# Kernel optimization log

Measured on AMD Instinct MI355X. Metric: run time of the kernel, lower is better.

## Reference

```python
import jax, jax.numpy as jnp
import numpy as np

N_EXPERTS = 8
D_MODEL = 1024
D_FF = 2048
N_TOKENS = 4096
TOP_K = 2


def _init_expert_weight(key, shape):
    # matches torch init: bound = sqrt(3) * (sqrt(1/3)/sqrt(fan_in)) = 1/sqrt(fan_in)
    fan_in = shape[1]
    bound = 1.0 / np.sqrt(fan_in)
    return jax.random.uniform(key, shape, dtype=jnp.float32, minval=-bound, maxval=bound)


def setup_inputs() -> dict:
    key = jax.random.key(0)
    k_x, k_idx, k_w, k1, k2, k3 = jax.random.split(key, 6)
    x = jax.random.normal(k_x, (N_TOKENS, D_MODEL), dtype=jnp.float32)
    expert_indices = jax.random.randint(k_idx, (N_TOKENS, TOP_K), 0, N_EXPERTS)
    expert_weights = jax.random.uniform(k_w, (N_TOKENS, TOP_K), dtype=jnp.float32)
    w1 = _init_expert_weight(k1, (N_EXPERTS, D_MODEL, D_FF))
    w2 = _init_expert_weight(k2, (N_EXPERTS, D_MODEL, D_FF))
    w3 = _init_expert_weight(k3, (N_EXPERTS, D_FF, D_MODEL))
    return {"x": x, "expert_indices": expert_indices, "expert_weights": expert_weights,
            "w1": w1, "w2": w2, "w3": w3}


def reference(x, expert_indices, expert_weights, w1, w2, w3):
    # SwiGLU per expert, computed densely over all (token, expert) pairs,
    # then the top-k selected expert outputs are gathered and combined.
    # Mathematically identical to the padded-bmm dispatch/combine in the source.
    gate = jax.nn.silu(jnp.einsum('td,edf->tef', x, w1))   # [T, E, F]
    value = jnp.einsum('td,edf->tef', x, w2)               # [T, E, F]
    hidden = gate * value                                  # [T, E, F]
    out_e = jnp.einsum('tef,efd->ted', hidden, w3)         # [T, E, D]
    # gather each token's top-k expert outputs: [T, K, D]
    sel = jnp.take_along_axis(out_e, expert_indices[:, :, None], axis=1)
    return jnp.sum(sel * expert_weights[:, :, None], axis=1)  # [T, D]
```

## Files before the change

### kernel.cpp

```cpp
#include <hip/hip_runtime.h>
#include <hip/hip_bf16.h>

#define N_TOK   4096
#define DM      1024
#define DF      2048
#define NEXP    8
#define NPAIR   (N_TOK * 2)
#define BM      128
#define BN      128
#define BK      32

typedef __attribute__((ext_vector_type(8))) short bf16x8;
typedef __attribute__((ext_vector_type(4))) float f32x4;

__device__ __forceinline__ unsigned short to_bf16(float f) {
    unsigned u = __builtin_bit_cast(unsigned, f);
    unsigned r = (u + 0x7FFFu + ((u >> 16) & 1u)) >> 16;
    return (unsigned short)r;
}
__device__ __forceinline__ unsigned pk_bf16(float a, float b) {
    return (unsigned)to_bf16(a) | ((unsigned)to_bf16(b) << 16);
}
__device__ __forceinline__ void gld16(const unsigned short* g, unsigned short* l) {
    __builtin_amdgcn_global_load_lds(
        (const __attribute__((address_space(1))) unsigned int*)(g),
        (__attribute__((address_space(3))) unsigned int*)(l), 16, 0, 0);
}

__global__ void k_count(const int* __restrict__ eidx, int* __restrict__ meta) {
    int i = blockIdx.x * 256 + threadIdx.x;
    if (i < NPAIR) atomicAdd(&meta[eidx[i] & 7], 1);
}
__global__ void k_scan(int* __restrict__ meta) {
    if (threadIdx.x == 0) {
        int off = 0, mt = 0;
        for (int e = 0; e < NEXP; ++e) {
            meta[16 + e] = off; meta[25 + e] = mt;
            int c = meta[e];
            off += c; mt += (c + BM - 1) / BM;
        }
        meta[16 + NEXP] = off; meta[25 + NEXP] = mt; meta[34] = mt;
    }
}
__global__ void k_scatter(const int* __restrict__ eidx, int* __restrict__ meta,
                          int* __restrict__ rows) {
    int i = blockIdx.x * 256 + threadIdx.x;
    if (i < NPAIR) {
        int e = eidx[i] & 7;
        int p = meta[16 + e] + atomicAdd(&meta[8 + e], 1);
        rows[p] = i;
    }
}

__global__ __launch_bounds__(256)
void k_cvt_x(const float* __restrict__ x, unsigned short* __restrict__ xb) {
    int i = (blockIdx.x * 256 + threadIdx.x) * 8;
    float4 v0 = *(const float4*)(x + i);
    float4 v1 = *(const float4*)(x + i + 4);
    uint4 w;
    w.x = pk_bf16(v0.x, v0.y); w.y = pk_bf16(v0.z, v0.w);
    w.z = pk_bf16(v1.x, v1.y); w.w = pk_bf16(v1.z, v1.w);
    *(uint4*)(xb + i) = w;
}

__global__ __launch_bounds__(256)
void k_transpose(const float* __restrict__ src, unsigned short* __restrict__ dst,
                 int K, int F) {
    __shared__ __align__(16) unsigned short tile[64 * 80];
    const int e  = blockIdx.z;
    const int k0 = blockIdx.y * 64;
    const int f0 = blockIdx.x * 64;
    const int t  = threadIdx.x;
    const float* s = src + (size_t)e * K * F;
    unsigned short* d = dst + (size_t)e * K * F;
    const int fi = t & 63;
    const int kg = t >> 6;
    #pragma unroll
    for (int i = 0; i < 16; ++i) {
        int k = kg * 16 + i;
        tile[k * 80 + fi] = to_bf16(s[(size_t)(k0 + k) * F + f0 + fi]);
    }
    __syncthreads();
    const int kc = (t & 7) * 8;
    const int fo = t >> 3;
    #pragma unroll
    for (int j = 0; j < 2; ++j) {
        int f = fo + j * 32;
        unsigned short v[8];
        #pragma unroll
        for (int i = 0; i < 8; ++i) v[i] = tile[(kc + i) * 80 + f];
        uint4 w;
        w.x = (unsigned)v[0] | ((unsigned)v[1] << 16);
        w.y = (unsigned)v[2] | ((unsigned)v[3] << 16);
        w.z = (unsigned)v[4] | ((unsigned)v[5] << 16);
        w.w = (unsigned)v[6] | ((unsigned)v[7] << 16);
        *(uint4*)&d[(size_t)(f0 + f) * K + k0 + kc] = w;
    }
}

__global__ __launch_bounds__(256, 2)
void k_gemm1_bf(const unsigned short* __restrict__ xb,
                const unsigned short* __restrict__ w1t,
                const unsigned short* __restrict__ w2t,
                const int* __restrict__ meta,
                const int* __restrict__ rows,
                unsigned short* __restrict__ H)
{
    __shared__ __align__(16) unsigned short L[3][12288];
    __shared__ int s_tok[BM];

    const int mt = blockIdx.y;
    if (mt >= meta[34]) return;
    int e = 0;
    #pragma unroll
    for (int i = 0; i < NEXP - 1; ++i) if (mt >= meta[25 + i + 1]) e = i + 1;
    const int rowEnd = meta[16 + e + 1];
    const int row0   = meta[16 + e] + (mt - meta[25 + e]) * BM;
    const int f0     = blockIdx.x * BN;
    const int tid    = threadIdx.x;

    if (tid < BM) {
        int gr = row0 + tid;
        s_tok[tid] = (gr < rowEnd) ? (rows[gr] >> 1) : 0;
    }
    __syncthreads();

    const int lane = tid & 63;
    const int wave = tid >> 6;
    const int r0 = wave * 32 + (lane >> 2);
    const int r1 = r0 + 16;
    const int kb = (lane & 3) * 8;
    const unsigned short* a_src0 = xb + (size_t)s_tok[r0] * DM + kb;
    const unsigned short* a_src1 = xb + (size_t)s_tok[r1] * DM + kb;
    const size_t wb = (size_t)e * DM * DF;
    const unsigned short* b1_src0 = w1t + wb + (size_t)(f0 + r0) * DM + kb;
    const unsigned short* b1_src1 = w1t + wb + (size_t)(f0 + r1) * DM + kb;
    const unsigned short* b2_src0 = w2t + wb + (size_t)(f0 + r0) * DM + kb;
    const unsigned short* b2_src1 = w2t + wb + (size_t)(f0 + r1) * DM + kb;

    f32x4 accg[4][4], accv[4][4];
    #pragma unroll
    for (int i = 0; i < 4; ++i)
        #pragma unroll
        for (int j = 0; j < 4; ++j) { accg[i][j] = (f32x4)0.f; accv[i][j] = (f32x4)0.f; }

    const int wm = (wave >> 1) * 64;
    const int wn = (wave & 1) * 64;
    const int am = lane & 15;
    const int ak = (lane >> 4) * 8;

    auto stage = [&](int b, int k0) {
        unsigned short* base = &L[b][0] + wave * 1024;
        gld16(a_src0  + k0, base);
        gld16(a_src1  + k0, base + 512);
        gld16(b1_src0 + k0, base + 4096);
        gld16(b1_src1 + k0, base + 4608);
        gld16(b2_src0 + k0, base + 8192);
        gld16(b2_src1 + k0, base + 8704);
    };
    auto compute = [&](int b) {
        const unsigned short* Ab = &L[b][0];
        bf16x8 a[4], b1[4], b2[4];
        #pragma unroll
        for (int mi = 0; mi < 4; ++mi)
            a[mi] = *(const bf16x8*)&Ab[(wm + mi * 16 + am) * BK + ak];
        #pragma unroll
        for (int ni = 0; ni < 4; ++ni) {
            b1[ni] = *(const bf16x8*)&Ab[4096 + (wn + ni * 16 + am) * BK + ak];
            b2[ni] = *(const bf16x8*)&Ab[8192 + (wn + ni * 16 + am) * BK + ak];
        }
        #pragma unroll
        for (int mi = 0; mi < 4; ++mi)
            #pragma unroll
            for (int ni = 0; ni < 4; ++ni) {
                accg[mi][ni] = __builtin_amdgcn_mfma_f32_16x16x32_bf16(a[mi], b1[ni], accg[mi][ni], 0, 0, 0);
                accv[mi][ni] = __builtin_amdgcn_mfma_f32_16x16x32_bf16(a[mi], b2[ni], accv[mi][ni], 0, 0, 0);
            }
    };

    stage(0, 0);
    stage(1, BK);
    for (int t = 0; t < DM / BK; ++t) {
        const int b = t % 3;
        if (t < DM / BK - 2) {
            stage((t + 2) % 3, (t + 2) * BK);
            asm volatile("s_waitcnt vmcnt(12)" ::: "memory");
        } else if (t == DM / BK - 2) {
            asm volatile("s_waitcnt vmcnt(6)" ::: "memory");
        } else {
            asm volatile("s_waitcnt vmcnt(0)" ::: "memory");
        }
        __builtin_amdgcn_s_barrier();
        __builtin_amdgcn_sched_barrier(0);
        compute(b);
        __builtin_amdgcn_sched_barrier(0);
        __builtin_amdgcn_s_barrier();
    }

    const int cn = lane & 15;
    const int cq = (lane >> 4) * 4;
    #pragma unroll
    for (int mi = 0; mi < 4; ++mi) {
        #pragma unroll
        for (int r = 0; r < 4; ++r) {
            const int row = wm + mi * 16 + cq + r;
            const int gr  = row0 + row;
            if (gr < rowEnd) {
                unsigned short* dst = H + (size_t)gr * DF + f0 + wn;
                #pragma unroll
                for (int ni = 0; ni < 4; ++ni) {
                    float g = accg[mi][ni][r];
                    float v = accv[mi][ni][r];
                    float h = (g * v) / (1.f + __expf(-g));
                    dst[ni * 16 + cn] = to_bf16(h);
                }
            }
        }
    }
}

__global__ __launch_bounds__(256, 2)
void k_gemm2_bf(const unsigned short* __restrict__ H,
                const unsigned short* __restrict__ w3t,
                const int* __restrict__ meta,
                const int* __restrict__ rows,
                const float* __restrict__ ew,
                float* __restrict__ out)
{
    __shared__ __align__(16) unsigned short L[3][8192];
    __shared__ int   s_tok[BM];
    __shared__ float s_w[BM];

    const int mt = blockIdx.y;
    if (mt >= meta[34]) return;
    int e = 0;
    #pragma unroll
    for (int i = 0; i < NEXP - 1; ++i) if (mt >= meta[25 + i + 1]) e = i + 1;
    const int rowEnd = meta[16 + e + 1];
    const int row0   = meta[16 + e] + (mt - meta[25 + e]) * BM;
    const int d0     = blockIdx.x * BN;
    const int tid    = threadIdx.x;

    if (tid < BM) {
        int gr = row0 + tid;
        if (gr < rowEnd) { int pr = rows[gr]; s_tok[tid] = pr >> 1; s_w[tid] = ew[pr]; }
        else             { s_tok[tid] = 0;    s_w[tid] = 0.f; }
    }
    __syncthreads();

    const int lane = tid & 63;
    const int wave = tid >> 6;
    const int r0 = wave * 32 + (lane >> 2);
    const int r1 = r0 + 16;
    const int kb = (lane & 3) * 8;
    int gr0 = row0 + r0; if (gr0 > NPAIR - 1) gr0 = NPAIR - 1;
    int gr1 = row0 + r1; if (gr1 > NPAIR - 1) gr1 = NPAIR - 1;
    const unsigned short* a_src0 = H + (size_t)gr0 * DF + kb;
    const unsigned short* a_src1 = H + (size_t)gr1 * DF + kb;
    const size_t wb = (size_t)e * DM * DF;
    const unsigned short* b_src0 = w3t + wb + (size_t)(d0 + r0) * DF + kb;
    const unsigned short* b_src1 = w3t + wb + (size_t)(d0 + r1) * DF + kb;

    f32x4 acc[4][4];
    #pragma unroll
    for (int i = 0; i < 4; ++i)
        #pragma unroll
        for (int j = 0; j < 4; ++j) acc[i][j] = (f32x4)0.f;

    const int wm = (wave >> 1) * 64;
    const int wn = (wave & 1) * 64;
    const int am = lane & 15;
    const int ak = (lane >> 4) * 8;

    auto stage = [&](int b, int k0) {
        unsigned short* base = &L[b][0] + wave * 1024;
        gld16(a_src0 + k0, base);
        gld16(a_src1 + k0, base + 512);
        gld16(b_src0 + k0, base + 4096);
        gld16(b_src1 + k0, base + 4608);
    };
    auto compute = [&](int b) {
        const unsigned short* Ab = &L[b][0];
        bf16x8 a[4], bfr[4];
        #pragma unroll
        for (int mi = 0; mi < 4; ++mi)
            a[mi] = *(const bf16x8*)&Ab[(wm + mi * 16 + am) * BK + ak];
        #pragma unroll
        for (int ni = 0; ni < 4; ++ni)
            bfr[ni] = *(const bf16x8*)&Ab[4096 + (wn + ni * 16 + am) * BK + ak];
        #pragma unroll
        for (int mi = 0; mi < 4; ++mi)
            #pragma unroll
            for (int ni = 0; ni < 4; ++ni)
                acc[mi][ni] = __builtin_amdgcn_mfma_f32_16x16x32_bf16(a[mi], bfr[ni], acc[mi][ni], 0, 0, 0);
    };

    stage(0, 0);
    stage(1, BK);
    for (int t = 0; t < DF / BK; ++t) {
        const int b = t % 3;
        if (t < DF / BK - 2) {
            stage((t + 2) % 3, (t + 2) * BK);
            asm volatile("s_waitcnt vmcnt(8)" ::: "memory");
        } else if (t == DF / BK - 2) {
            asm volatile("s_waitcnt vmcnt(4)" ::: "memory");
        } else {
            asm volatile("s_waitcnt vmcnt(0)" ::: "memory");
        }
        __builtin_amdgcn_s_barrier();
        __builtin_amdgcn_sched_barrier(0);
        compute(b);
        __builtin_amdgcn_sched_barrier(0);
        __builtin_amdgcn_s_barrier();
    }

    const int cn = lane & 15;
    const int cq = (lane >> 4) * 4;
    #pragma unroll
    for (int mi = 0; mi < 4; ++mi) {
        #pragma unroll
        for (int r = 0; r < 4; ++r) {
            const int row = wm + mi * 16 + cq + r;
            const int gr  = row0 + row;
            if (gr < rowEnd) {
                const int   tok = s_tok[row];
                const float wgt = s_w[row];
                float* dst = out + (size_t)tok * DM + d0 + wn;
                #pragma unroll
                for (int ni = 0; ni < 4; ++ni)
                    atomicAdd(&dst[ni * 16 + cn], wgt * acc[mi][ni][r]);
            }
        }
    }
}

__global__ __launch_bounds__(256)
void k_fallback(const float* __restrict__ x, const int* __restrict__ eidx,
                const float* __restrict__ ew, const float* __restrict__ w1,
                const float* __restrict__ w2, const float* __restrict__ w3,
                float* __restrict__ out)
{
    __shared__ float xs[DM];
    __shared__ float hs[DF];
    const int pair = blockIdx.x;
    const int t = pair >> 1;
    const int e = eidx[pair] & 7;
    const float wgt = ew[pair];
    const int tid = threadIdx.x;
    for (int i = tid; i < DM; i += 256) xs[i] = x[(size_t)t * DM + i];
    __syncthreads();
    for (int f = tid; f < DF; f += 256) {
        const float* c1 = w1 + (size_t)e * DM * DF + f;
        const float* c2 = w2 + (size_t)e * DM * DF + f;
        float g = 0.f, v = 0.f;
        for (int d = 0; d < DM; ++d) {
            float xv = xs[d];
            g += xv * c1[(size_t)d * DF];
            v += xv * c2[(size_t)d * DF];
        }
        hs[f] = (g * v) / (1.f + __expf(-g));
    }
    __syncthreads();
    for (int d = tid; d < DM; d += 256) {
        const float* c3 = w3 + (size_t)e * DF * DM + d;
        float o = 0.f;
        for (int f = 0; f < DF; ++f) o += hs[f] * c3[(size_t)f * DM];
        atomicAdd(&out[(size_t)t * DM + d], wgt * o);
    }
}

extern "C" void kernel_launch(void* const* d_in, const int* in_sizes, int n_in,
                              void* d_out, int out_size, void* d_ws, size_t ws_size,
                              hipStream_t stream)
{
    const float* x  = (const float*)d_in[0];
    const int*   ei = (const int*)  d_in[1];
    const float* ew = (const float*)d_in[2];
    const float* w1 = (const float*)d_in[3];
    const float* w2 = (const float*)d_in[4];
    const float* w3 = (const float*)d_in[5];
    float* out = (float*)d_out;

    (void)hipMemsetAsync(d_out, 0, (size_t)out_size * sizeof(float), stream);

    const size_t SZ_H  = (size_t)NPAIR * DF * 2;
    const size_t SZ_XB = (size_t)N_TOK * DM * 2;
    const size_t SZ_W  = (size_t)NEXP * DM * DF * 2;
    const size_t OFF_H  = 65536;
    const size_t OFF_XB = OFF_H + SZ_H;
    const size_t OFF_W1 = OFF_XB + SZ_XB;
    const size_t OFF_W2 = OFF_W1 + SZ_W;
    const size_t OFF_W3 = OFF_W2 + SZ_W;
    const size_t NEED_BIG = OFF_W3 + SZ_W;

    if (ws_size < NEED_BIG) {
        k_fallback<<<NPAIR, 256, 0, stream>>>(x, ei, ew, w1, w2, w3, out);
        return;
    }

    int* meta = (int*)d_ws;
    int* rows = meta + 64;
    unsigned short* H   = (unsigned short*)((char*)d_ws + OFF_H);
    unsigned short* xb  = (unsigned short*)((char*)d_ws + OFF_XB);
    unsigned short* w1t = (unsigned short*)((char*)d_ws + OFF_W1);
    unsigned short* w2t = (unsigned short*)((char*)d_ws + OFF_W2);
    unsigned short* w3t = (unsigned short*)((char*)d_ws + OFF_W3);

    (void)hipMemsetAsync(d_ws, 0, 64, stream);
    k_count  <<<NPAIR / 256, 256, 0, stream>>>(ei, meta);
    k_scan   <<<1, 64, 0, stream>>>(meta);
    k_scatter<<<NPAIR / 256, 256, 0, stream>>>(ei, meta, rows);

    k_cvt_x<<<(N_TOK * DM) / 2048, 256, 0, stream>>>(x, xb);
    k_transpose<<<dim3(DF / 64, DM / 64, NEXP), 256, 0, stream>>>(w1, w1t, DM, DF);
    k_transpose<<<dim3(DF / 64, DM / 64, NEXP), 256, 0, stream>>>(w2, w2t, DM, DF);
    k_transpose<<<dim3(DM / 64, DF / 64, NEXP), 256, 0, stream>>>(w3, w3t, DF, DM);

    const int NMT = NPAIR / BM + NEXP;
    k_gemm1_bf<<<dim3(DF / BN, NMT), 256, 0, stream>>>(xb, w1t, w2t, meta, rows, H);
    k_gemm2_bf<<<dim3(DM / BN, NMT), 256, 0, stream>>>(H, w3t, meta, rows, ew, out);
}
```

Before: 500.4 us.

## Fuse routing and conversion kernels, remap GEMM tiles per XCD, drop triple-buffering

```diff
diff --git a/kernel.cpp b/kernel.cpp
--- a/kernel.cpp
+++ b/kernel.cpp
@@ -27,50 +27,41 @@
         (__attribute__((address_space(3))) unsigned int*)(l), 16, 0, 0);
 }
 
-__global__ void k_count(const int* __restrict__ eidx, int* __restrict__ meta) {
-    int i = blockIdx.x * 256 + threadIdx.x;
-    if (i < NPAIR) atomicAdd(&meta[eidx[i] & 7], 1);
-}
-__global__ void k_scan(int* __restrict__ meta) {
-    if (threadIdx.x == 0) {
+__global__ __launch_bounds__(1024)
+void k_sort(const int* __restrict__ eidx, int* __restrict__ meta,
+            int* __restrict__ rows) {
+    __shared__ int cnt[NEXP];
+    __shared__ int cur[NEXP];
+    const int tid = threadIdx.x;
+    if (tid < NEXP) cnt[tid] = 0;
+    __syncthreads();
+    #pragma unroll
+    for (int i = tid; i < NPAIR; i += 1024) atomicAdd(&cnt[eidx[i] & 7], 1);
+    __syncthreads();
+    if (tid == 0) {
         int off = 0, mt = 0;
         for (int e = 0; e < NEXP; ++e) {
-            meta[16 + e] = off; meta[25 + e] = mt;
-            int c = meta[e];
+            meta[16 + e] = off; meta[25 + e] = mt; cur[e] = off;
+            int c = cnt[e];
             off += c; mt += (c + BM - 1) / BM;
         }
         meta[16 + NEXP] = off; meta[25 + NEXP] = mt; meta[34] = mt;
     }
-}
-__global__ void k_scatter(const int* __restrict__ eidx, int* __restrict__ meta,
-                          int* __restrict__ rows) {
-    int i = blockIdx.x * 256 + threadIdx.x;
-    if (i < NPAIR) {
+    __syncthreads();
+    #pragma unroll
+    for (int i = tid; i < NPAIR; i += 1024) {
         int e = eidx[i] & 7;
-        int p = meta[16 + e] + atomicAdd(&meta[8 + e], 1);
+        int p = atomicAdd(&cur[e], 1);
         rows[p] = i;
     }
 }
 
-__global__ __launch_bounds__(256)
-void k_cvt_x(const float* __restrict__ x, unsigned short* __restrict__ xb) {
-    int i = (blockIdx.x * 256 + threadIdx.x) * 8;
-    float4 v0 = *(const float4*)(x + i);
-    float4 v1 = *(const float4*)(x + i + 4);
-    uint4 w;
-    w.x = pk_bf16(v0.x, v0.y); w.y = pk_bf16(v0.z, v0.w);
-    w.z = pk_bf16(v1.x, v1.y); w.w = pk_bf16(v1.z, v1.w);
-    *(uint4*)(xb + i) = w;
-}
-
-__global__ __launch_bounds__(256)
-void k_transpose(const float* __restrict__ src, unsigned short* __restrict__ dst,
-                 int K, int F) {
-    __shared__ __align__(16) unsigned short tile[64 * 80];
-    const int e  = blockIdx.z;
-    const int k0 = blockIdx.y * 64;
-    const int f0 = blockIdx.x * 64;
-    const int t  = threadIdx.x;
+__device__ __forceinline__ void d_transpose(const float* __restrict__ src,
+                                            unsigned short* __restrict__ dst,
+                                            int K, int F, int e, int bx, int by,
+                                            unsigned short* tile, int t) {
+    const int k0 = by * 64;
+    const int f0 = bx * 64;
     const float* s = src + (size_t)e * K * F;
     unsigned short* d = dst + (size_t)e * K * F;
     const int fi = t & 63;
@@ -96,6 +87,51 @@
         w.w = (unsigned)v[6] | ((unsigned)v[7] << 16);
         *(uint4*)&d[(size_t)(f0 + f) * K + k0 + kc] = w;
     }
+}
+
+__global__ __launch_bounds__(256)
+void k_prepass(const float* __restrict__ x, unsigned short* __restrict__ xb,
+               const float* __restrict__ w1, unsigned short* __restrict__ w1t,
+               const float* __restrict__ w2, unsigned short* __restrict__ w2t,
+               const float* __restrict__ w3, unsigned short* __restrict__ w3t) {
+    __shared__ __align__(16) unsigned short tile[64 * 80];
+    const int b = blockIdx.x;
+    const int t = threadIdx.x;
+    if (b < 2048) {
+        int i = (b * 256 + t) * 8;
+        float4 v0 = *(const float4*)(x + i);
+        float4 v1 = *(const float4*)(x + i + 4);
+        uint4 w;
+        w.x = pk_bf16(v0.x, v0.y); w.y = pk_bf16(v0.z, v0.w);
+        w.z = pk_bf16(v1.x, v1.y); w.w = pk_bf16(v1.z, v1.w);
+        *(uint4*)(xb + i) = w;
+    } else if (b < 6144) {
+        int l = b - 2048;
+        int e = l >> 9, rem = l & 511;
+        d_transpose(w1, w1t, DM, DF, e, rem & 31, rem >> 5, tile, t);
+    } else if (b < 10240) {
+        int l = b - 6144;
+        int e = l >> 9, rem = l & 511;
+        d_transpose(w2, w2t, DM, DF, e, rem & 31, rem >> 5, tile, t);
+    } else {
+        int l = b - 10240;
+        int e = l >> 9, rem = l & 511;
+        d_transpose(w3, w3t, DF, DM, e, rem & 15, rem >> 4, tile, t);
+    }
+}
+
+__device__ __forceinline__ bool xcd_map(const int* meta, int bid, int ngroups,
+                                        int& mt, int& ng) {
+    const int MT = meta[34];
+    const int x = bid & 7;
+    const int j = bid >> 3;
+    const int q = MT >> 3, r = MT & 7;
+    const int Sx = q + (x < r ? 1 : 0);
+    if (Sx == 0 || j >= Sx * ngroups) return false;
+    ng = j / Sx;
+    const int mtl = j - ng * Sx;
+    mt = x * q + (x < r ? x : r) + mtl;
+    return true;
 }
 
 __global__ __launch_bounds__(256, 2)
@@ -106,17 +142,19 @@
                 const int* __restrict__ rows,
                 unsigned short* __restrict__ H)
 {
-    __shared__ __align__(16) unsigned short L[3][12288];
+    __shared__ __align__(16) unsigned short As [BM * BK];
+    __shared__ __align__(16) unsigned short B1s[BN * BK];
+    __shared__ __align__(16) unsigned short B2s[BN * BK];
     __shared__ int s_tok[BM];
 
-    const int mt = blockIdx.y;
-    if (mt >= meta[34]) return;
+    int mt, ng;
+    if (!xcd_map(meta, blockIdx.x, DF / BN, mt, ng)) return;
     int e = 0;
     #pragma unroll
     for (int i = 0; i < NEXP - 1; ++i) if (mt >= meta[25 + i + 1]) e = i + 1;
     const int rowEnd = meta[16 + e + 1];
     const int row0   = meta[16 + e] + (mt - meta[25 + e]) * BM;
-    const int f0     = blockIdx.x * BN;
+    const int f0     = ng * BN;
     const int tid    = threadIdx.x;
 
     if (tid < BM) {
@@ -137,6 +175,12 @@
     const unsigned short* b1_src1 = w1t + wb + (size_t)(f0 + r1) * DM + kb;
     const unsigned short* b2_src0 = w2t + wb + (size_t)(f0 + r0) * DM + kb;
     const unsigned short* b2_src1 = w2t + wb + (size_t)(f0 + r1) * DM + kb;
+    unsigned short* As0  = &As [wave * 1024];
+    unsigned short* As1  = &As [wave * 1024 + 512];
+    unsigned short* B1s0 = &B1s[wave * 1024];
+    unsigned short* B1s1 = &B1s[wave * 1024 + 512];
+    unsigned short* B2s0 = &B2s[wave * 1024];
+    unsigned short* B2s1 = &B2s[wave * 1024 + 512];
 
     f32x4 accg[4][4], accv[4][4];
     #pragma unroll
@@ -149,25 +193,22 @@
     const int am = lane & 15;
     const int ak = (lane >> 4) * 8;
 
-    auto stage = [&](int b, int k0) {
-        unsigned short* base = &L[b][0] + wave * 1024;
-        gld16(a_src0  + k0, base);
-        gld16(a_src1  + k0, base + 512);
-        gld16(b1_src0 + k0, base + 4096);
-        gld16(b1_src1 + k0, base + 4608);
-        gld16(b2_src0 + k0, base + 8192);
-        gld16(b2_src1 + k0, base + 8704);
-    };
-    auto compute = [&](int b) {
-        const unsigned short* Ab = &L[b][0];
+    for (int k0 = 0; k0 < DM; k0 += BK) {
+        gld16(a_src0 + k0, As0);
+        gld16(a_src1 + k0, As1);
+        gld16(b1_src0 + k0, B1s0);
+        gld16(b1_src1 + k0, B1s1);
+        gld16(b2_src0 + k0, B2s0);
+        gld16(b2_src1 + k0, B2s1);
+        __syncthreads();
+
         bf16x8 a[4], b1[4], b2[4];
         #pragma unroll
-        for (int mi = 0; mi < 4; ++mi)
-            a[mi] = *(const bf16x8*)&Ab[(wm + mi * 16 + am) * BK + ak];
+        for (int mi = 0; mi < 4; ++mi) a[mi] = *(const bf16x8*)&As[(wm + mi * 16 + am) * BK + ak];
         #pragma unroll
         for (int ni = 0; ni < 4; ++ni) {
-            b1[ni] = *(const bf16x8*)&Ab[4096 + (wn + ni * 16 + am) * BK + ak];
-            b2[ni] = *(const bf16x8*)&Ab[8192 + (wn + ni * 16 + am) * BK + ak];
+            b1[ni] = *(const bf16x8*)&B1s[(wn + ni * 16 + am) * BK + ak];
+            b2[ni] = *(const bf16x8*)&B2s[(wn + ni * 16 + am) * BK + ak];
         }
         #pragma unroll
         for (int mi = 0; mi < 4; ++mi)
@@ -176,25 +217,7 @@
                 accg[mi][ni] = __builtin_amdgcn_mfma_f32_16x16x32_bf16(a[mi], b1[ni], accg[mi][ni], 0, 0, 0);
                 accv[mi][ni] = __builtin_amdgcn_mfma_f32_16x16x32_bf16(a[mi], b2[ni], accv[mi][ni], 0, 0, 0);
             }
-    };
-
-    stage(0, 0);
-    stage(1, BK);
-    for (int t = 0; t < DM / BK; ++t) {
-        const int b = t % 3;
-        if (t < DM / BK - 2) {
-            stage((t + 2) % 3, (t + 2) * BK);
-            asm volatile("s_waitcnt vmcnt(12)" ::: "memory");
-        } else if (t == DM / BK - 2) {
-            asm volatile("s_waitcnt vmcnt(6)" ::: "memory");
-        } else {
-            asm volatile("s_waitcnt vmcnt(0)" ::: "memory");
-        }
-        __builtin_amdgcn_s_barrier();
-        __builtin_amdgcn_sched_barrier(0);
-        compute(b);
-        __builtin_amdgcn_sched_barrier(0);
-        __builtin_amdgcn_s_barrier();
+        __syncthreads();
     }
 
     const int cn = lane & 15;
@@ -227,18 +250,19 @@
                 const float* __restrict__ ew,
                 float* __restrict__ out)
 {
-    __shared__ __align__(16) unsigned short L[3][8192];
+    __shared__ __align__(16) unsigned short As[BM * BK];
+    __shared__ __align__(16) unsigned short Bs[BN * BK];
     __shared__ int   s_tok[BM];
     __shared__ float s_w[BM];
 
-    const int mt = blockIdx.y;
-    if (mt >= meta[34]) return;
+    int mt, ng;
+    if (!xcd_map(meta, blockIdx.x, DM / BN, mt, ng)) return;
     int e = 0;
     #pragma unroll
     for (int i = 0; i < NEXP - 1; ++i) if (mt >= meta[25 + i + 1]) e = i + 1;
     const int rowEnd = meta[16 + e + 1];
     const int row0   = meta[16 + e] + (mt - meta[25 + e]) * BM;
-    const int d0     = blockIdx.x * BN;
+    const int d0     = ng * BN;
     const int tid    = threadIdx.x;
 
     if (tid < BM) {
@@ -260,6 +284,10 @@
     const size_t wb = (size_t)e * DM * DF;
     const unsigned short* b_src0 = w3t + wb + (size_t)(d0 + r0) * DF + kb;
     const unsigned short* b_src1 = w3t + wb + (size_t)(d0 + r1) * DF + kb;
+    unsigned short* As0 = &As[wave * 1024];
+    unsigned short* As1 = &As[wave * 1024 + 512];
+    unsigned short* Bs0 = &Bs[wave * 1024];
+    unsigned short* Bs1 = &Bs[wave * 1024 + 512];
 
     f32x4 acc[4][4];
     #pragma unroll
@@ -272,46 +300,24 @@
     const int am = lane & 15;
     const int ak = (lane >> 4) * 8;
 
-    auto stage = [&](int b, int k0) {
-        unsigned short* base = &L[b][0] + wave * 1024;
-        gld16(a_src0 + k0, base);
-        gld16(a_src1 + k0, base + 512);
-        gld16(b_src0 + k0, base + 4096);
-        gld16(b_src1 + k0, base + 4608);
-    };
-    auto compute = [&](int b) {
-        const unsigned short* Ab = &L[b][0];
-        bf16x8 a[4], bfr[4];
-        #pragma unroll
-        for (int mi = 0; mi < 4; ++mi)
-            a[mi] = *(const bf16x8*)&Ab[(wm + mi * 16 + am) * BK + ak];
-        #pragma unroll
-        for (int ni = 0; ni < 4; ++ni)
-            bfr[ni] = *(const bf16x8*)&Ab[4096 + (wn + ni * 16 + am) * BK + ak];
+    for (int k0 = 0; k0 < DF; k0 += BK) {
+        gld16(a_src0 + k0, As0);
+        gld16(a_src1 + k0, As1);
+        gld16(b_src0 + k0, Bs0);
+        gld16(b_src1 + k0, Bs1);
+        __syncthreads();
+
+        bf16x8 a[4], b[4];
+        #pragma unroll
+        for (int mi = 0; mi < 4; ++mi) a[mi] = *(const bf16x8*)&As[(wm + mi * 16 + am) * BK + ak];
+        #pragma unroll
+        for (int ni = 0; ni < 4; ++ni) b[ni] = *(const bf16x8*)&Bs[(wn + ni * 16 + am) * BK + ak];
         #pragma unroll
         for (int mi = 0; mi < 4; ++mi)
             #pragma unroll
             for (int ni = 0; ni < 4; ++ni)
-                acc[mi][ni] = __builtin_amdgcn_mfma_f32_16x16x32_bf16(a[mi], bfr[ni], acc[mi][ni], 0, 0, 0);
-    };
-
-    stage(0, 0);
-    stage(1, BK);
-    for (int t = 0; t < DF / BK; ++t) {
-        const int b = t % 3;
-        if (t < DF / BK - 2) {
-            stage((t + 2) % 3, (t + 2) * BK);
-            asm volatile("s_waitcnt vmcnt(8)" ::: "memory");
-        } else if (t == DF / BK - 2) {
-            asm volatile("s_waitcnt vmcnt(4)" ::: "memory");
-        } else {
-            asm volatile("s_waitcnt vmcnt(0)" ::: "memory");
-        }
-        __builtin_amdgcn_s_barrier();
-        __builtin_amdgcn_sched_barrier(0);
-        compute(b);
-        __builtin_amdgcn_sched_barrier(0);
-        __builtin_amdgcn_s_barrier();
+                acc[mi][ni] = __builtin_amdgcn_mfma_f32_16x16x32_bf16(a[mi], b[ni], acc[mi][ni], 0, 0, 0);
+        __syncthreads();
     }
 
     const int cn = lane & 15;
@@ -406,17 +412,9 @@
     unsigned short* w2t = (unsigned short*)((char*)d_ws + OFF_W2);
     unsigned short* w3t = (unsigned short*)((char*)d_ws + OFF_W3);
 
-    (void)hipMemsetAsync(d_ws, 0, 64, stream);
-    k_count  <<<NPAIR / 256, 256, 0, stream>>>(ei, meta);
-    k_scan   <<<1, 64, 0, stream>>>(meta);
-    k_scatter<<<NPAIR / 256, 256, 0, stream>>>(ei, meta, rows);
-
-    k_cvt_x<<<(N_TOK * DM) / 2048, 256, 0, stream>>>(x, xb);
-    k_transpose<<<dim3(DF / 64, DM / 64, NEXP), 256, 0, stream>>>(w1, w1t, DM, DF);
-    k_transpose<<<dim3(DF / 64, DM / 64, NEXP), 256, 0, stream>>>(w2, w2t, DM, DF);
-    k_transpose<<<dim3(DM / 64, DF / 64, NEXP), 256, 0, stream>>>(w3, w3t, DF, DM);
-
-    const int NMT = NPAIR / BM + NEXP;
-    k_gemm1_bf<<<dim3(DF / BN, NMT), 256, 0, stream>>>(xb, w1t, w2t, meta, rows, H);
-    k_gemm2_bf<<<dim3(DM / BN, NMT), 256, 0, stream>>>(H, w3t, meta, rows, ew, out);
-}
+    k_sort<<<1, 1024, 0, stream>>>(ei, meta, rows);
+    k_prepass<<<14336, 256, 0, stream>>>(x, xb, w1, w1t, w2, w2t, w3, w3t);
+
+    k_gemm1_bf<<<1152, 256, 0, stream>>>(xb, w1t, w2t, meta, rows, H);
+    k_gemm2_bf<<<640, 256, 0, stream>>>(H, w3t, meta, rows, ew, out);
+}
```

After: 419.0 us. 1.19x faster.
